# Optimization experiments

Measured on AMD Instinct MI355X. Metric: run time of the kernel, lower is better.

## Reference

```python
import jax, jax.numpy as jnp
import numpy as np

SCALE = 1000.0
NEG = -1000000000.0
B, S, T, E, H = 64, 512, 96, 256, 512  # batch, src_len, trg_len, embed_dim, hidden_dim
ENC_DIM = 2 * H


def setup_inputs() -> dict:
    key = jax.random.key(0)
    def rn(i, shape):
        return jax.random.normal(jax.random.fold_in(key, i), shape, jnp.float32) / np.sqrt(shape[-1])
    inp = {}
    inp["src"] = jax.random.uniform(jax.random.fold_in(key, 100), (B, S), jnp.float32, 50.0, 1500.0)
    src_len = jax.random.randint(jax.random.fold_in(key, 101), (B,), S // 2, S + 1)
    inp["src_mask"] = (jnp.arange(S)[None, :] < src_len[:, None]).astype(jnp.int32)
    trg = jax.random.uniform(jax.random.fold_in(key, 102), (B, T), jnp.float32, 50.0, 1500.0)
    inp["trg"] = trg.at[:, 0].set(0.0)  # position 0 is the start sentinel
    trg_len = jax.random.randint(jax.random.fold_in(key, 103), (B,), T // 2, T + 1)
    inp["trg_mask"] = (jnp.arange(T)[None, :] < trg_len[:, None]).astype(jnp.int32)
    shapes = {
        "enc_proj_W": (E, 1), "enc_proj_b": (E,),
        "enc_Wih_f": (4 * H, E), "enc_Whh_f": (4 * H, H), "enc_bih_f": (4 * H,), "enc_bhh_f": (4 * H,),
        "enc_Wih_b": (4 * H, E), "enc_Whh_b": (4 * H, H), "enc_bih_b": (4 * H,), "enc_bhh_b": (4 * H,),
        "fc_h_W": (H, 2 * H), "fc_h_b": (H,), "fc_c_W": (H, 2 * H), "fc_c_b": (H,),
        "dec_proj_W": (E, 1), "dec_proj_b": (E,),
        "attn_Wenc": (H, ENC_DIM), "attn_Wdec": (H, H), "attn_v": (1, H),
        "dec_Wih": (4 * H, E + ENC_DIM), "dec_Whh": (4 * H, H), "dec_bih": (4 * H,), "dec_bhh": (4 * H,),
        "val_W": (1, H + ENC_DIM + E), "val_b": (1,),
        "stop_W": (1, H + ENC_DIM + E), "stop_b": (1,),
    }
    for i, (name, shp) in enumerate(shapes.items()):
        inp[name] = rn(i, shp)
    return inp


def _lstm_scan(x_tbe, m_tb1, Wih, Whh, bih, bhh, reverse):
    # Mask-gated LSTM scan == pack_padded_sequence semantics (padding at end):
    # state is frozen and outputs zeroed at padded steps; reverse=True gives the
    # backward direction of the bidirectional encoder.
    b, h = x_tbe.shape[1], Whh.shape[1]
    init = (jnp.zeros((b, h), x_tbe.dtype), jnp.zeros((b, h), x_tbe.dtype))
    bias = bih + bhh
    def step(carry, xm):
        hprev, cprev = carry
        xt, m = xm
        gates = xt @ Wih.T + hprev @ Whh.T + bias  # [B,4H], torch gate order i,f,g,o
        i, f, g, o = jnp.split(gates, 4, axis=-1)
        c_new = jax.nn.sigmoid(f) * cprev + jax.nn.sigmoid(i) * jnp.tanh(g)
        h_new = jax.nn.sigmoid(o) * jnp.tanh(c_new)
        hn = jnp.where(m, h_new, hprev)
        cn = jnp.where(m, c_new, cprev)
        return (hn, cn), jnp.where(m, h_new, 0.0)
    (hT, cT), outs = jax.lax.scan(step, init, (x_tbe, m_tb1), reverse=reverse)
    return outs, hT, cT


def _forward(src, trg, enc_proj_W, enc_proj_b, enc_Wih_f, enc_Whh_f, enc_bih_f, enc_bhh_f, enc_Wih_b, enc_Whh_b, enc_bih_b, enc_bhh_b, fc_h_W, fc_h_b, fc_c_W, fc_c_b, dec_proj_W, dec_proj_b, attn_Wenc, attn_Wdec, attn_v, dec_Wih, dec_Whh, dec_bih, dec_bhh, val_W, val_b, stop_W, stop_b, src_mask, trg_mask):
    src_norm = src / SCALE
    # ---- encoder (bidirectional, n_layers=1, dropout inactive in eval) ----
    emb = src_norm[..., None] * enc_proj_W[:, 0] + enc_proj_b  # Linear(1,E) -> [B,S,E]
    emb_t = jnp.transpose(emb, (1, 0, 2))                      # [S,B,E] time-major
    m_t = (src_mask.T > 0)[..., None]                          # [S,B,1]
    out_f, hF, cF = _lstm_scan(emb_t, m_t, enc_Wih_f, enc_Whh_f, enc_bih_f, enc_bhh_f, False)
    out_b, hB, cB = _lstm_scan(emb_t, m_t, enc_Wih_b, enc_Whh_b, enc_bih_b, enc_bhh_b, True)
    enc_outputs = jnp.transpose(jnp.concatenate([out_f, out_b], -1), (1, 0, 2))  # [B,S,2H]
    hidden = jnp.tanh(jnp.concatenate([hF, hB], -1) @ fc_h_W.T + fc_h_b)  # [B,H]
    cell = jnp.tanh(jnp.concatenate([cF, cB], -1) @ fc_c_W.T + fc_c_b)    # [B,H]
    # ---- decoder loop (full teacher forcing, ratio=1.0) ----
    eh = enc_outputs @ attn_Wenc.T  # [B,S,H], loop-invariant (same math, hoisted)
    valid = src_mask > 0            # [B,S]
    dec_bias = dec_bih + dec_bhh
    def dec_step(carry, x_t):
        h, c = carry
        energy = jnp.tanh((h @ attn_Wdec.T)[:, None, :] + eh)  # [B,S,H]
        scores = jnp.where(valid, energy @ attn_v[0], NEG)     # [B,S]
        w = jax.nn.softmax(scores, axis=1)
        context = jnp.einsum('bs,bse->be', w, enc_outputs)     # [B,2H]
        e = x_t[:, None] * dec_proj_W[:, 0] + dec_proj_b       # [B,E]
        gates = jnp.concatenate([e, context], -1) @ dec_Wih.T + h @ dec_Whh.T + dec_bias
        i, f, g, o = jnp.split(gates, 4, axis=-1)
        c_new = jax.nn.sigmoid(f) * c + jax.nn.sigmoid(i) * jnp.tanh(g)
        h_new = jax.nn.sigmoid(o) * jnp.tanh(c_new)
        feat = jnp.concatenate([h_new, context, e], -1)        # [B, H+2H+E]
        pv = feat @ val_W[0] + val_b[0]
        sl = feat @ stop_W[0] + stop_b[0]
        return (h_new, c_new), (pv * SCALE, sl)
    dec_in = (trg[:, :-1] / SCALE).T  # [T-1,B]: inputs for steps t=1..trg_len-1
    _, (pred_values, stop_logits) = jax.lax.scan(dec_step, (hidden, cell), dec_in)
    return pred_values.T, stop_logits.T  # each [B, T-1]


def reference(src, src_mask, trg, trg_mask, enc_proj_W, enc_proj_b, enc_Wih_f, enc_Whh_f, enc_bih_f, enc_bhh_f, enc_Wih_b, enc_Whh_b, enc_bih_b, enc_bhh_b, fc_h_W, fc_h_b, fc_c_W, fc_c_b, dec_proj_W, dec_proj_b, attn_Wenc, attn_Wdec, attn_v, dec_Wih, dec_Whh, dec_bih, dec_bhh, val_W, val_b, stop_W, stop_b):
    return _forward(src, trg, enc_proj_W, enc_proj_b, enc_Wih_f, enc_Whh_f, enc_bih_f, enc_bhh_f, enc_Wih_b, enc_Whh_b, enc_bih_b, enc_bhh_b, fc_h_W, fc_h_b, fc_c_W, fc_c_b, dec_proj_W, dec_proj_b, attn_Wenc, attn_Wdec, attn_v, dec_Wih, dec_Whh, dec_bih, dec_bhh, val_W, val_b, stop_W, stop_b, src_mask, trg_mask)
```

## Files before the change

kernel.cpp:

```cpp
#include <hip/hip_runtime.h>
#include <hip/hip_bf16.h>

#define AGENT __HIP_MEMORY_SCOPE_AGENT

typedef float f32x4 __attribute__((ext_vector_type(4)));
typedef short short8 __attribute__((ext_vector_type(8)));
union V16 { f32x4 f; short8 s; };


__device__ __forceinline__ float sigm(float x){ return 1.f/(1.f+__expf(-x)); }
__device__ __forceinline__ float tanhfast(float x){
  float ax = fabsf(x);
  float e = __expf(-2.f*ax);
  float r = (1.f-e)/(1.f+e);
  return copysignf(r, x);
}
__device__ __forceinline__ float dot4(float4 a, float4 b){
  return fmaf(a.x,b.x, fmaf(a.y,b.y, fmaf(a.z,b.z, a.w*b.w)));
}
__device__ __forceinline__ unsigned short bfbits(float x){
  return __bfloat16_as_ushort(__float2bfloat16(x));
}
__device__ __forceinline__ float bfu2f(unsigned short u){
  union{unsigned v; float f;} x; x.v = ((unsigned)u)<<16; return x.f;
}

__global__ void __launch_bounds__(256) precompute(
  const float* __restrict__ Wenc,
  const float* __restrict__ Wihf, const float* __restrict__ epW, const float* __restrict__ epb,
  const float* __restrict__ bihf, const float* __restrict__ bhhf,
  const float* __restrict__ Wihb, const float* __restrict__ bihb, const float* __restrict__ bhhb,
  const float* __restrict__ dWih, const float* __restrict__ dpW, const float* __restrict__ dpb,
  const float* __restrict__ dbih, const float* __restrict__ dbhh,
  const float* __restrict__ valW, const float* __restrict__ valb,
  const float* __restrict__ stopW, const float* __restrict__ stopb,
  float* __restrict__ PQ, float* __restrict__ WT, float* __restrict__ hc)
{
  const int idx = blockIdx.x*256 + threadIdx.x;
  if (idx < 524288){
    const int j = idx >> 9, n = idx & 511;
    WT[idx] = Wenc[(size_t)n*1024 + j];
  } else if (idx < 524288 + 6*2048){
    const int q = idx - 524288;
    const int set = q >> 11, j = q & 2047;
    const float* row; const float* vec; float add = 0.f;
    switch(set){
      case 0: row = Wihf + (size_t)j*256; vec = epW; break;
      case 1: row = Wihf + (size_t)j*256; vec = epb; add = bihf[j]+bhhf[j]; break;
      case 2: row = Wihb + (size_t)j*256; vec = epW; break;
      case 3: row = Wihb + (size_t)j*256; vec = epb; add = bihb[j]+bhhb[j]; break;
      case 4: row = dWih + (size_t)j*1280; vec = dpW; break;
      default: row = dWih + (size_t)j*1280; vec = dpb; add = dbih[j]+dbhh[j]; break;
    }
    float a = add;
    for (int e=0;e<256;e++) a = fmaf(row[e], vec[e], a);
    PQ[set*2048 + j] = a;
  } else if (idx < 524288 + 6*2048 + 4){
    const int q = idx - (524288 + 6*2048);
    const float* wrow = (q<2) ? valW : stopW;
    const float* vec  = (q&1) ? dpb : dpW;
    float a = (q&1) ? ((q<2)? valb[0] : stopb[0]) : 0.f;
    for (int e=0;e<256;e++) a = fmaf(wrow[1536+e], vec[e], a);
    hc[q] = a;
  }
}

__global__ void __launch_bounds__(512) wconv(
  const float* __restrict__ Whhf, const float* __restrict__ Whhb,
  const float* __restrict__ dWih, const float* __restrict__ dWhh,
  const float* __restrict__ Wdec, const float* __restrict__ Wenc,
  unsigned short* __restrict__ Wbf, unsigned short* __restrict__ Wcat,
  unsigned short* __restrict__ Wdecb, unsigned short* __restrict__ Wencb)
{
  const int i = blockIdx.x*512 + threadIdx.x;
  if (i < 2097152){
    const float v = (i < 1048576) ? Whhf[i] : Whhb[i-1048576];
    Wbf[i] = bfbits(v);
  } else if (i < 2097152+3145728){
    const int q = i - 2097152;
    const int r = q/1536, k = q - r*1536;
    const float v = (k<1024) ? dWih[(size_t)r*1280 + 256 + k] : dWhh[(size_t)r*512 + (k-1024)];
    Wcat[q] = bfbits(v);
  } else if (i < 2097152+3145728+262144){
    const int q = i - (2097152+3145728);
    Wdecb[q] = bfbits(Wdec[q]);
  } else if (i < 2097152+3145728+262144+524288){
    const int q = i - (2097152+3145728+262144);
    Wencb[q] = bfbits(Wenc[q]);
  }
}

__global__ void __launch_bounds__(512) enc_mfma(
    const float* __restrict__ src, const int* __restrict__ smask,
    const unsigned short* __restrict__ Wbf,
    const float* __restrict__ PQ,
    unsigned short* __restrict__ hbuf,
    float* __restrict__ hfin,
    float* __restrict__ cf, float* __restrict__ cb,
    __hip_bfloat16* __restrict__ enc,
    unsigned* __restrict__ cnt)
{
  __shared__ float hlds[16*256];
  __shared__ float red[4*64*4];
  __shared__ float gbuf[4*256];
  __shared__ alignas(16) unsigned short hstage[256];
  __shared__ alignas(16) unsigned short estage[256];

  const int tid = threadIdx.x;
  const int bid = blockIdx.x;
  const int dir = bid>>7, bhalf = (bid>>5)&3, us = bid&31;
  const int b0 = bhalf*16;
  unsigned* gcnt = cnt + (dir*4 + bhalf)*32;
  const int wv = tid>>6, lane = tid&63;
  const int nt = wv&3, kh = wv>>2;
  const int rowb = lane&15;

  short8 bfr[8];
  {
    const int g = nt*512 + us*16 + (lane&15);
    const unsigned short* wp = Wbf + ((size_t)dir*2048 + g)*512 + kh*256 + (lane>>4)*8;
    #pragma unroll
    for (int kt=0;kt<8;kt++) bfr[kt] = *(const short8*)(wp + kt*32);
  }

  float p0=0,p1=0,p2=0,p3=0,q0=0,q1=0,q2=0,q3=0;
  float creg = 0.f, hprev = 0.f;
  int bg = 0, ug = 0;
  if (tid < 256){
    bg = b0 + (tid>>4);
    ug = us*16 + (tid&15);
    const float* P = PQ + dir*4096; const float* Q = P + 2048;
    p0=P[ug]; p1=P[ug+512]; p2=P[ug+1024]; p3=P[ug+1536];
    q0=Q[ug]; q1=Q[ug+512]; q2=Q[ug+1024]; q3=Q[ug+1536];
  }

  for (int tt=0; tt<512; ++tt){
    const int t = dir ? (511-tt) : tt;
    if (tt>0){
      if (tid==0){
        while (__hip_atomic_load(gcnt, __ATOMIC_RELAXED, AGENT) < 32u*(unsigned)tt)
          __builtin_amdgcn_s_sleep(1);
      }
      __syncthreads();
      const int par = (tt-1)&1;
      f32x4 tmp0, tmp1;
      {
        const int f0 = tid, f1 = 512 + tid;
        const unsigned short* g0 = hbuf + (((size_t)(dir*2+par)*64 + b0 + (f0>>6))<<9) + (f0&63)*8;
        const unsigned short* g1 = hbuf + (((size_t)(dir*2+par)*64 + b0 + (f1>>6))<<9) + (f1&63)*8;
        asm volatile("global_load_dwordx4 %0, %1, off sc0 sc1" : "=v"(tmp0) : "v"(g0) : "memory");
        asm volatile("global_load_dwordx4 %0, %1, off sc0 sc1" : "=v"(tmp1) : "v"(g1) : "memory");
      }
      asm volatile("s_waitcnt vmcnt(0)" ::: "memory");
      __builtin_amdgcn_sched_barrier(0);
      {
        const int r0 = tid>>6, c0 = tid&63;
        *(f32x4*)&hlds[r0*256 + ((c0 ^ (r0&7))<<2)] = tmp0;
        const int r1 = (512+tid)>>6, c1 = tid&63;
        *(f32x4*)&hlds[r1*256 + ((c1 ^ (r1&7))<<2)] = tmp1;
      }
      __syncthreads();
    }

    f32x4 acc = {0.f,0.f,0.f,0.f};
    if (tt>0){
      #pragma unroll
      for (int kt=0; kt<8; ++kt){
        const int ch = (kh*8 + kt)*4 + (lane>>4);
        V16 a; a.f = *(const f32x4*)&hlds[rowb*256 + ((ch ^ (rowb&7))<<2)];
        acc = __builtin_amdgcn_mfma_f32_16x16x32_bf16(a.s, bfr[kt], acc, 0, 0, 0);
      }
    }
    if (kh==1) *(f32x4*)&red[(nt*64+lane)*4] = acc;
    __syncthreads();
    if (kh==0){
      const f32x4 o = *(const f32x4*)&red[(nt*64+lane)*4];
      #pragma unroll
      for (int i=0;i<4;i++){
        const int r = (lane>>4)*4 + i, c = lane&15;
        gbuf[nt*256 + r*16 + c] = acc[i] + o[i];
      }
    }
    __syncthreads();

    if (tid < 256){
      const float sx = src[bg*512+t]*0.001f;
      const int m = smask[bg*512+t];
      const float gi = gbuf[0*256+tid] + sx*p0 + q0;
      const float gf = gbuf[1*256+tid] + sx*p1 + q1;
      const float gg = gbuf[2*256+tid] + sx*p2 + q2;
      const float go = gbuf[3*256+tid] + sx*p3 + q3;
      const float cn = fmaf(sigm(gf), creg, sigm(gi)*tanhfast(gg));
      const float hn = sigm(go)*tanhfast(cn);
      const float hk = m ? hn : hprev;
      creg = m ? cn : creg;
      hprev = hk;
      hstage[tid] = bfbits(hk);
      estage[tid] = bfbits(m ? hn : 0.f);
    }
    __syncthreads();
    if (tid < 32){
      const int row = tid>>1, hw = tid&1;
      const f32x4 v = *(const f32x4*)(hstage + row*16 + hw*8);
      unsigned short* dst = hbuf + (((size_t)(dir*2+(tt&1))*64 + b0 + row)<<9) + us*16 + hw*8;
      asm volatile("global_store_dwordx4 %0, %1, off sc0 sc1" :: "v"(dst), "v"(v) : "memory");
    } else if (tid < 64){
      const int j = tid-32, row = j>>1, hw = j&1;
      const f32x4 v = *(const f32x4*)(estage + row*16 + hw*8);
      *(f32x4*)((unsigned short*)enc + ((size_t)((b0+row)*512 + t))*1024 + dir*512 + us*16 + hw*8) = v;
    }
    asm volatile("s_waitcnt vmcnt(0)" ::: "memory");
    __syncthreads();
    if (tid==0) __hip_atomic_fetch_add(gcnt, 1u, __ATOMIC_RELAXED, AGENT);
  }

  if (tid < 256){
    hfin[dir*32768 + bg*512 + ug] = hprev;
    (dir ? cb : cf)[bg*512 + ug] = creg;
  }
}

__global__ void __launch_bounds__(256) fc_init(
  const float* __restrict__ hf0, const float* __restrict__ hb0,
  const float* __restrict__ cf, const float* __restrict__ cb,
  const float* __restrict__ fchW, const float* __restrict__ fchB,
  const float* __restrict__ fccW, const float* __restrict__ fccB,
  float* __restrict__ dech, float* __restrict__ decc)
{
  const int which = blockIdx.x >> 7;
  const int wid = blockIdx.x & 127;
  const int b = threadIdx.x >> 2, ul = threadIdx.x & 3;
  const int u = wid*4 + ul;
  const float* s0 = which ? cf : hf0;
  const float* s1 = which ? cb : hb0;
  const float* W = which ? fccW : fchW;
  float acc = (which ? fccB : fchB)[u];
  const float4* x0 = (const float4*)(s0 + b*512);
  const float4* x1 = (const float4*)(s1 + b*512);
  const float4* wr = (const float4*)(W + (size_t)u*1024);
  #pragma unroll 4
  for (int k=0;k<128;k++) acc += dot4(x0[k], wr[k]);
  #pragma unroll 4
  for (int k=0;k<128;k++) acc += dot4(x1[k], wr[128+k]);
  (which ? decc : dech)[b*512+u] = tanhfast(acc);
}

__global__ void __launch_bounds__(256) eh_mfma(
  const unsigned short* __restrict__ enc,
  const unsigned short* __restrict__ Wencb,
  unsigned short* __restrict__ eh2)
{
  const int b = blockIdx.x>>6, st = (blockIdx.x>>3)&7, nt0 = blockIdx.x&7;
  const int wv = threadIdx.x>>6, lane = threadIdx.x&63;
  const int sA = st*64 + wv*16 + (lane&15);
  const int kb = (lane>>4)*8;
  const unsigned short* ap  = enc + ((size_t)(b*512 + sA))*1024 + kb;
  const unsigned short* bp0 = Wencb + ((size_t)(nt0*64 + (lane&15)))*1024 + kb;
  f32x4 acc[4] = {{0,0,0,0},{0,0,0,0},{0,0,0,0},{0,0,0,0}};
  for (int k0=0; k0<1024; k0+=32){
    V16 a; a.f = *(const f32x4*)(ap + k0);
    #pragma unroll
    for (int nt=0; nt<4; ++nt){
      V16 bb; bb.f = *(const f32x4*)(bp0 + (size_t)nt*16*1024 + k0);
      acc[nt] = __builtin_amdgcn_mfma_f32_16x16x32_bf16(a.s, bb.s, acc[nt], 0, 0, 0);
    }
  }
  const int sO = st*64 + wv*16 + (lane>>4)*4;
  const int col = lane&15;
  #pragma unroll
  for (int nt=0; nt<4; ++nt){
    #pragma unroll
    for (int i=0;i<4;i++){
      eh2[((size_t)(b*512 + sO + i))*512 + nt0*64 + nt*16 + col] = bfbits(acc[nt][i]);
    }
  }
}

__global__ void __launch_bounds__(256) enc_tr(
  const unsigned short* __restrict__ enc, unsigned short* __restrict__ encT2)
{
  __shared__ unsigned short tl[64][80];
  const int b = blockIdx.x>>7, st = (blockIdx.x>>4)&7, jt = blockIdx.x&15;
  const int r = threadIdx.x>>2, q = threadIdx.x&3;
  const unsigned short* src = enc + ((size_t)(b*512 + st*64 + r))*1024 + jt*64 + q*16;
  *(short8*)&tl[r][q*16]   = *(const short8*)src;
  *(short8*)&tl[r][q*16+8] = *(const short8*)(src+8);
  __syncthreads();
  unsigned short tmp[16];
  #pragma unroll
  for (int e=0;e<16;e++) tmp[e] = tl[q*16+e][r];
  unsigned short* dst = encT2 + ((size_t)(b*1024 + jt*64 + r))*512 + st*64 + q*16;
  *(short8*)dst     = *(short8*)&tmp[0];
  *(short8*)(dst+8) = *(short8*)&tmp[8];
}

template<int NG>
__device__ __forceinline__ void gbar(unsigned* gctr, unsigned* root, int grp, unsigned gen){
  asm volatile("s_waitcnt vmcnt(0)" ::: "memory");
  __syncthreads();
  if (threadIdx.x==0){
    const unsigned old = __hip_atomic_fetch_add(gctr + grp*32, 1u, __ATOMIC_RELAXED, AGENT);
    if (old == gen*16u - 1u)
      __hip_atomic_fetch_add(root, 1u, __ATOMIC_RELAXED, AGENT);
    while (__hip_atomic_load(root, __ATOMIC_RELAXED, AGENT) < gen*(unsigned)NG)
      __builtin_amdgcn_s_sleep(1);
  }
  __syncthreads();
}
template<int NB>
__device__ __forceinline__ void mbar(unsigned* mc, unsigned mgen){
  asm volatile("s_waitcnt vmcnt(0)" ::: "memory");
  __syncthreads();
  if (threadIdx.x==0){
    __hip_atomic_fetch_add(mc, 1u, __ATOMIC_RELAXED, AGENT);
    while (__hip_atomic_load(mc, __ATOMIC_RELAXED, AGENT) < mgen*(unsigned)NB)
      __builtin_amdgcn_s_sleep(1);
  }
  __syncthreads();
}

__global__ void __launch_bounds__(512) dec_fused256(
  const float* __restrict__ trg, const int* __restrict__ smask,
  const float* __restrict__ attnv,
  const unsigned short* __restrict__ eh2,
  const unsigned short* __restrict__ encT2,
  const unsigned short* __restrict__ Wcat,
  const unsigned short* __restrict__ Wdecb,
  const float* __restrict__ PQd, const float* __restrict__ hc,
  const float* __restrict__ valW, const float* __restrict__ stopW,
  const float* __restrict__ dech0, const float* __restrict__ decc0,
  float* __restrict__ scorep, float* __restrict__ ctxf,
  unsigned short* __restrict__ xbuf, float* __restrict__ gates,
  float* __restrict__ hcur, float* __restrict__ out,
  unsigned* __restrict__ gctr, unsigned* __restrict__ root, unsigned* __restrict__ mctr)
{
  __shared__ alignas(16) float redl[8192];
  __shared__ float vlds[512];
  __shared__ float hldsa[512];
  __shared__ float adhl[128];
  __shared__ float wlds[512];
  const int tid = threadIdx.x;
  const int bid = blockIdx.x;
  const int b = bid>>2, quad = bid&3;
  const int grp = bid>>4;
  const int lane = tid&63, wv = tid>>6;
  unsigned* mc = mctr + b*32;
  unsigned g = 0, m = 0;

  vlds[tid] = attnv[tid];

  short8 gw[6];
  if (bid < 128){
    const int n = bid*16 + (lane&15);
    const unsigned short* wp = Wcat + (size_t)n*1536 + wv*192 + (lane>>4)*8;
    #pragma unroll
    for (int ks=0;ks<6;ks++) gw[ks] = *(const short8*)(wp + ks*32);
  }

  const bool isb = (quad==0);
  float hr=0.f, cr=0.f;
  float pqi=0,pqf=0,pqg=0,pqo=0, qqi=0,qqf=0,qqg=0,qqo=0;
  float vwh=0,vwc0=0,vwc1=0, swh=0,swc0=0,swc1=0;
  if (isb){
    hr = dech0[b*512+tid]; cr = decc0[b*512+tid];
    pqi = PQd[tid];      pqf = PQd[512+tid];      pqg = PQd[1024+tid];      pqo = PQd[1536+tid];
    qqi = PQd[2048+tid]; qqf = PQd[2048+512+tid]; qqg = PQd[2048+1024+tid]; qqo = PQd[2048+1536+tid];
    vwh = valW[tid]; vwc0 = valW[512+tid]; vwc1 = valW[1024+tid];
    swh = stopW[tid]; swc0 = stopW[512+tid]; swc1 = stopW[1024+tid];
  }

  if (isb){
    const unsigned hb16 = (unsigned)bfbits(hr);
    unsigned short* xp = xbuf + b*1536 + 1024 + tid;
    asm volatile("global_store_short %0, %1, off sc0 sc1" :: "v"(xp), "v"(hb16) : "memory");
    float* hp = hcur + b*512 + tid;
    asm volatile("global_store_dword %0, %1, off sc0 sc1" :: "v"(hp), "v"(hr) : "memory");
  }
  ++m; mbar<4>(mc, m);

  for (int t=0; t<95; ++t){
    {
      float hv; const float* hp = hcur + b*512 + tid;
      asm volatile("global_load_dword %0, %1, off sc0 sc1\ns_waitcnt vmcnt(0)" : "=v"(hv) : "v"(hp) : "memory");
      hldsa[tid] = hv;
      __syncthreads();
      {
        const int jl = tid>>2, uc = tid&3;
        const unsigned short* wp = Wdecb + (size_t)(quad*128 + jl)*512 + uc*128;
        float a = 0.f;
        #pragma unroll
        for (int i=0;i<16;i++){
          const short8 w8 = *(const short8*)(wp + i*8);
          #pragma unroll
          for (int e=0;e<8;e++)
            a = fmaf(hldsa[uc*128 + i*8 + e], bfu2f((unsigned short)w8[e]), a);
        }
        redl[tid] = a;
      }
      __syncthreads();
      if (tid < 128)
        adhl[tid] = redl[tid*4] + redl[tid*4+1] + redl[tid*4+2] + redl[tid*4+3];
      __syncthreads();
      {
        const unsigned short* ep = eh2 + ((size_t)(b*512 + tid))*512 + quad*128;
        float part = 0.f;
        #pragma unroll
        for (int i=0;i<16;i++){
          const short8 e8 = *(const short8*)(ep + i*8);
          #pragma unroll
          for (int e=0;e<8;e++){
            const int n = i*8 + e;
            part = fmaf(vlds[quad*128+n], tanhfast(adhl[n] + bfu2f((unsigned short)e8[e])), part);
          }
        }
        float* sp = scorep + (size_t)bid*512 + tid;
        asm volatile("global_store_dword %0, %1, off sc0 sc1" :: "v"(sp), "v"(part) : "memory");
      }
    }
    ++m; mbar<4>(mc, m);

    {
      float pa, pb, pc, pd;
      const float* pp = scorep + (size_t)(b*4)*512 + tid;
      asm volatile("global_load_dword %0, %1, off sc0 sc1" : "=v"(pa) : "v"(pp) : "memory");
      asm volatile("global_load_dword %0, %1, off sc0 sc1" : "=v"(pb) : "v"(pp+512) : "memory");
      asm volatile("global_load_dword %0, %1, off sc0 sc1" : "=v"(pc) : "v"(pp+1024) : "memory");
      asm volatile("global_load_dword %0, %1, off sc0 sc1" : "=v"(pd) : "v"(pp+1536) : "memory");
      asm volatile("s_waitcnt vmcnt(0)" ::: "memory");
      __builtin_amdgcn_sched_barrier(0);
      float s0 = (pa+pb)+(pc+pd);
      s0 = smask[b*512+tid] ? s0 : -1.0e9f;
      redl[512+tid] = s0;
      __syncthreads();
      for (int off=256; off>0; off>>=1){
        if (tid<off) redl[512+tid] = fmaxf(redl[512+tid], redl[512+tid+off]);
        __syncthreads();
      }
      const float mx = redl[512];
      __syncthreads();
      const float e = __expf(s0 - mx);
      redl[512+tid] = e;
      __syncthreads();
      for (int off=256; off>0; off>>=1){
        if (tid<off) redl[512+tid] += redl[512+tid+off];
        __syncthreads();
      }
      const float Z = redl[512];
      __syncthreads();
      wlds[tid] = e / Z;
      __syncthreads();
      {
        const int jj = tid>>1, sh = tid&1;
        const unsigned short* cp = encT2 + ((size_t)(b*1024 + quad*256 + jj))*512 + sh*256;
        float c = 0.f;
        #pragma unroll
        for (int i=0;i<32;i++){
          const short8 c8 = *(const short8*)(cp + i*8);
          #pragma unroll
          for (int e2=0;e2<8;e2++)
            c = fmaf(wlds[sh*256 + i*8 + e2], bfu2f((unsigned short)c8[e2]), c);
        }
        redl[tid] = c;
      }
      __syncthreads();
      if (tid < 256){
        const float cv = redl[tid*2] + redl[tid*2+1];
        const int j = quad*256 + tid;
        float* cp2 = ctxf + b*1024 + j;
        asm volatile("global_store_dword %0, %1, off sc0 sc1" :: "v"(cp2), "v"(cv) : "memory");
        const unsigned cb16 = (unsigned)bfbits(cv);
        unsigned short* xp = xbuf + b*1536 + j;
        asm volatile("global_store_short %0, %1, off sc0 sc1" :: "v"(xp), "v"(cb16) : "memory");
      }
    }
    ++g; gbar<16>(gctr, root, grp, g);

    if (bid < 128){
      f32x4 av[2][6];
      f32x4 acc[4] = {{0,0,0,0},{0,0,0,0},{0,0,0,0},{0,0,0,0}};
      {
        const unsigned short* xp0 = xbuf + (size_t)(lane&15)*1536 + wv*192 + (lane>>4)*8;
        #pragma unroll
        for (int ks=0;ks<6;ks++){
          const unsigned short* p = xp0 + ks*32;
          asm volatile("global_load_dwordx4 %0, %1, off sc0 sc1" : "=v"(av[0][ks]) : "v"(p) : "memory");
        }
      }
      #pragma unroll
      for (int mt=0; mt<4; ++mt){
        if (mt<3){
          const unsigned short* xpn = xbuf + (size_t)((mt+1)*16 + (lane&15))*1536 + wv*192 + (lane>>4)*8;
          #pragma unroll
          for (int ks=0;ks<6;ks++){
            const unsigned short* p = xpn + ks*32;
            asm volatile("global_load_dwordx4 %0, %1, off sc0 sc1" : "=v"(av[(mt+1)&1][ks]) : "v"(p) : "memory");
          }
          asm volatile("s_waitcnt vmcnt(6)" ::: "memory");
        } else {
          asm volatile("s_waitcnt vmcnt(0)" ::: "memory");
        }
        __builtin_amdgcn_sched_barrier(0);
        #pragma unroll
        for (int ks=0;ks<6;ks++){
          V16 a; a.f = av[mt&1][ks];
          acc[mt] = __builtin_amdgcn_mfma_f32_16x16x32_bf16(a.s, gw[ks], acc[mt], 0, 0, 0);
        }
      }
      #pragma unroll
      for (int mt=0; mt<4; ++mt)
        *(f32x4*)&redl[wv*1024 + lane*16 + mt*4] = acc[mt];
    }
    __syncthreads();
    if (bid < 128){
      #pragma unroll
      for (int h2=0; h2<2; ++h2){
        const int o = h2*512 + tid;
        const int ob = o>>4, col = o&15;
        const int mt = ob>>4, row = ob&15;
        const int base = (((row>>2)<<4) | col)*16 + mt*4 + (row&3);
        float gsum = 0.f;
        #pragma unroll
        for (int w2=0; w2<8; ++w2) gsum += redl[w2*1024 + base];
        float* gp = gates + ob*2048 + bid*16 + col;
        asm volatile("global_store_dword %0, %1, off sc0 sc1" :: "v"(gp), "v"(gsum) : "memory");
      }
    }
    ++g; gbar<16>(gctr, root, grp, g);

    if (isb){
      float g4[4], c0v, c1v;
      {
        const float* gp = gates + b*2048 + tid;
        const float* cp = ctxf + b*1024 + tid;
        asm volatile("global_load_dword %0, %1, off sc0 sc1" : "=v"(g4[0]) : "v"(gp) : "memory");
        asm volatile("global_load_dword %0, %1, off sc0 sc1" : "=v"(g4[1]) : "v"(gp+512) : "memory");
        asm volatile("global_load_dword %0, %1, off sc0 sc1" : "=v"(g4[2]) : "v"(gp+1024) : "memory");
        asm volatile("global_load_dword %0, %1, off sc0 sc1" : "=v"(g4[3]) : "v"(gp+1536) : "memory");
        asm volatile("global_load_dword %0, %1, off sc0 sc1" : "=v"(c0v) : "v"(cp) : "memory");
        asm volatile("global_load_dword %0, %1, off sc0 sc1" : "=v"(c1v) : "v"(cp+512) : "memory");
        asm volatile("s_waitcnt vmcnt(0)" ::: "memory");
        __builtin_amdgcn_sched_barrier(0);
      }
      const float x = trg[b*96 + t]*0.001f;
      const float gi = g4[0] + x*pqi + qqi;
      const float gf = g4[1] + x*pqf + qqf;
      const float gg = g4[2] + x*pqg + qqg;
      const float go = g4[3] + x*pqo + qqo;
      const float cn = fmaf(sigm(gf), cr, sigm(gi)*tanhfast(gg));
      const float hn = sigm(go)*tanhfast(cn);
      cr = cn; hr = hn;
      const unsigned hb16 = (unsigned)bfbits(hn);
      unsigned short* xp = xbuf + b*1536 + 1024 + tid;
      asm volatile("global_store_short %0, %1, off sc0 sc1" :: "v"(xp), "v"(hb16) : "memory");
      float* hp = hcur + b*512 + tid;
      asm volatile("global_store_dword %0, %1, off sc0 sc1" :: "v"(hp), "v"(hn) : "memory");
      redl[512+tid]  = fmaf(hn, vwh, fmaf(c0v, vwc0, c1v*vwc1));
      redl[1024+tid] = fmaf(hn, swh, fmaf(c0v, swc0, c1v*swc1));
      __syncthreads();
      for (int off=256; off>0; off>>=1){
        if (tid<off){ redl[512+tid]+=redl[512+tid+off]; redl[1024+tid]+=redl[1024+tid+off]; }
        __syncthreads();
      }
      if (tid==0){
        out[b*95 + t] = (redl[512] + x*hc[0] + hc[1])*1000.f;
        out[6080 + b*95 + t] = redl[1024] + x*hc[2] + hc[3];
      }
    }
    ++m; mbar<4>(mc, m);
  }
}

__global__ void __launch_bounds__(512, 4) dec_fused512(
  const float* __restrict__ trg, const int* __restrict__ smask,
  const float* __restrict__ attnv,
  const unsigned short* __restrict__ eh2,
  const unsigned short* __restrict__ encT2,
  const unsigned short* __restrict__ Wcat,
  const unsigned short* __restrict__ Wdecb,
  const float* __restrict__ PQd, const float* __restrict__ hc,
  const float* __restrict__ valW, const float* __restrict__ stopW,
  const float* __restrict__ dech0, const float* __restrict__ decc0,
  float* __restrict__ scorep, float* __restrict__ ctxf,
  unsigned short* __restrict__ xbuf, float* __restrict__ gates,
  float* __restrict__ hcur, float* __restrict__ out,
  unsigned* __restrict__ gctr, unsigned* __restrict__ root, unsigned* __restrict__ mctr)
{
  __shared__ alignas(16) float redl[8192];
  __shared__ float vlds[512];
  __shared__ float hldsa[512];
  __shared__ float adhl[64];
  __shared__ float wlds[512];
  const int tid = threadIdx.x;
  const int bid = blockIdx.x;
  const int b = bid>>3, oct = bid&7;
  const int grp = bid>>4;
  const int lane = tid&63, wv = tid>>6;
  unsigned* mc = mctr + b*32;
  unsigned g = 0, m = 0;

  vlds[tid] = attnv[tid];

  short8 gw[6];
  if (bid < 128){
    const int n = bid*16 + (lane&15);
    const unsigned short* wp = Wcat + (size_t)n*1536 + wv*192 + (lane>>4)*8;
    #pragma unroll
    for (int ks=0;ks<6;ks++) gw[ks] = *(const short8*)(wp + ks*32);
  }

  const bool isb = (oct==0);
  float hr=0.f, cr=0.f;
  float pqi=0,pqf=0,pqg=0,pqo=0, qqi=0,qqf=0,qqg=0,qqo=0;
  float vwh=0,vwc0=0,vwc1=0, swh=0,swc0=0,swc1=0;
  if (isb){
    hr = dech0[b*512+tid]; cr = decc0[b*512+tid];
    pqi = PQd[tid];      pqf = PQd[512+tid];      pqg = PQd[1024+tid];      pqo = PQd[1536+tid];
    qqi = PQd[2048+tid]; qqf = PQd[2048+512+tid]; qqg = PQd[2048+1024+tid]; qqo = PQd[2048+1536+tid];
    vwh = valW[tid]; vwc0 = valW[512+tid]; vwc1 = valW[1024+tid];
    swh = stopW[tid]; swc0 = stopW[512+tid]; swc1 = stopW[1024+tid];
  }

  if (isb){
    const unsigned hb16 = (unsigned)bfbits(hr);
    unsigned short* xp = xbuf + b*1536 + 1024 + tid;
    asm volatile("global_store_short %0, %1, off sc0 sc1" :: "v"(xp), "v"(hb16) : "memory");
    float* hp = hcur + b*512 + tid;
    asm volatile("global_store_dword %0, %1, off sc0 sc1" :: "v"(hp), "v"(hr) : "memory");
  }
  ++m; mbar<8>(mc, m);

  for (int t=0; t<95; ++t){
    {
      float hv; const float* hp = hcur + b*512 + tid;
      asm volatile("global_load_dword %0, %1, off sc0 sc1\ns_waitcnt vmcnt(0)" : "=v"(hv) : "v"(hp) : "memory");
      hldsa[tid] = hv;
      __syncthreads();
      {
        const int jl = tid>>3, uc = tid&7;
        const unsigned short* wp = Wdecb + (size_t)(oct*64 + jl)*512 + uc*64;
        float a = 0.f;
        #pragma unroll
        for (int i=0;i<8;i++){
          const short8 w8 = *(const short8*)(wp + i*8);
          #pragma unroll
          for (int e=0;e<8;e++)
            a = fmaf(hldsa[uc*64 + i*8 + e], bfu2f((unsigned short)w8[e]), a);
        }
        redl[tid] = a;
      }
      __syncthreads();
      if (tid < 64){
        float s8 = 0.f;
        #pragma unroll
        for (int i=0;i<8;i++) s8 += redl[tid*8+i];
        adhl[tid] = s8;
      }
      __syncthreads();
      {
        const unsigned short* ep = eh2 + ((size_t)(b*512 + tid))*512 + oct*64;
        float part = 0.f;
        #pragma unroll
        for (int i=0;i<8;i++){
          const short8 e8 = *(const short8*)(ep + i*8);
          #pragma unroll
          for (int e=0;e<8;e++){
            const int n = i*8 + e;
            part = fmaf(vlds[oct*64+n], tanhfast(adhl[n] + bfu2f((unsigned short)e8[e])), part);
          }
        }
        float* sp = scorep + (size_t)bid*512 + tid;
        asm volatile("global_store_dword %0, %1, off sc0 sc1" :: "v"(sp), "v"(part) : "memory");
      }
    }
    ++m; mbar<8>(mc, m);

    {
      float ps[8];
      const float* pp = scorep + (size_t)(b*8)*512 + tid;
      #pragma unroll
      for (int i=0;i<8;i++){
        const float* p = pp + i*512;
        asm volatile("global_load_dword %0, %1, off sc0 sc1" : "=v"(ps[i]) : "v"(p) : "memory");
      }
      asm volatile("s_waitcnt vmcnt(0)" ::: "memory");
      __builtin_amdgcn_sched_barrier(0);
      float s0 = ((ps[0]+ps[1])+(ps[2]+ps[3]))+((ps[4]+ps[5])+(ps[6]+ps[7]));
      s0 = smask[b*512+tid] ? s0 : -1.0e9f;
      redl[512+tid] = s0;
      __syncthreads();
      for (int off=256; off>0; off>>=1){
        if (tid<off) redl[512+tid] = fmaxf(redl[512+tid], redl[512+tid+off]);
        __syncthreads();
      }
      const float mx = redl[512];
      __syncthreads();
      const float e = __expf(s0 - mx);
      redl[512+tid] = e;
      __syncthreads();
      for (int off=256; off>0; off>>=1){
        if (tid<off) redl[512+tid] += redl[512+tid+off];
        __syncthreads();
      }
      const float Z = redl[512];
      __syncthreads();
      wlds[tid] = e / Z;
      __syncthreads();
      {
        const int jj = tid>>2, sh = tid&3;
        const unsigned short* cp = encT2 + ((size_t)(b*1024 + oct*128 + jj))*512 + sh*128;
        float c = 0.f;
        #pragma unroll
        for (int i=0;i<16;i++){
          const short8 c8 = *(const short8*)(cp + i*8);
          #pragma unroll
          for (int e2=0;e2<8;e2++)
            c = fmaf(wlds[sh*128 + i*8 + e2], bfu2f((unsigned short)c8[e2]), c);
        }
        redl[tid] = c;
      }
      __syncthreads();
      if (tid < 128){
        const float cv = redl[tid*4] + redl[tid*4+1] + redl[tid*4+2] + redl[tid*4+3];
        const int j = oct*128 + tid;
        float* cp2 = ctxf + b*1024 + j;
        asm volatile("global_store_dword %0, %1, off sc0 sc1" :: "v"(cp2), "v"(cv) : "memory");
        const unsigned cb16 = (unsigned)bfbits(cv);
        unsigned short* xp = xbuf + b*1536 + j;
        asm volatile("global_store_short %0, %1, off sc0 sc1" :: "v"(xp), "v"(cb16) : "memory");
      }
    }
    ++g; gbar<32>(gctr, root, grp, g);

    if (bid < 128){
      f32x4 av[2][6];
      f32x4 acc[4] = {{0,0,0,0},{0,0,0,0},{0,0,0,0},{0,0,0,0}};
      {
        const unsigned short* xp0 = xbuf + (size_t)(lane&15)*1536 + wv*192 + (lane>>4)*8;
        #pragma unroll
        for (int ks=0;ks<6;ks++){
          const unsigned short* p = xp0 + ks*32;
          asm volatile("global_load_dwordx4 %0, %1, off sc0 sc1" : "=v"(av[0][ks]) : "v"(p) : "memory");
        }
      }
      #pragma unroll
      for (int mt=0; mt<4; ++mt){
        if (mt<3){
          const unsigned short* xpn = xbuf + (size_t)((mt+1)*16 + (lane&15))*1536 + wv*192 + (lane>>4)*8;
          #pragma unroll
          for (int ks=0;ks<6;ks++){
            const unsigned short* p = xpn + ks*32;
            asm volatile("global_load_dwordx4 %0, %1, off sc0 sc1" : "=v"(av[(mt+1)&1][ks]) : "v"(p) : "memory");
          }
          asm volatile("s_waitcnt vmcnt(6)" ::: "memory");
        } else {
          asm volatile("s_waitcnt vmcnt(0)" ::: "memory");
        }
        __builtin_amdgcn_sched_barrier(0);
        #pragma unroll
        for (int ks=0;ks<6;ks++){
          V16 a; a.f = av[mt&1][ks];
          acc[mt] = __builtin_amdgcn_mfma_f32_16x16x32_bf16(a.s, gw[ks], acc[mt], 0, 0, 0);
        }
      }
      #pragma unroll
      for (int mt=0; mt<4; ++mt)
        *(f32x4*)&redl[wv*1024 + lane*16 + mt*4] = acc[mt];
    }
    __syncthreads();
    if (bid < 128){
      #pragma unroll
      for (int h2=0; h2<2; ++h2){
        const int o = h2*512 + tid;
        const int ob = o>>4, col = o&15;
        const int mt = ob>>4, row = ob&15;
        const int base = (((row>>2)<<4) | col)*16 + mt*4 + (row&3);
        float gsum = 0.f;
        #pragma unroll
        for (int w2=0; w2<8; ++w2) gsum += redl[w2*1024 + base];
        float* gp = gates + ob*2048 + bid*16 + col;
        asm volatile("global_store_dword %0, %1, off sc0 sc1" :: "v"(gp), "v"(gsum) : "memory");
      }
    }
    ++g; gbar<32>(gctr, root, grp, g);

    if (isb){
      float g4[4], c0v, c1v;
      {
        const float* gp = gates + b*2048 + tid;
        const float* cp = ctxf + b*1024 + tid;
        asm volatile("global_load_dword %0, %1, off sc0 sc1" : "=v"(g4[0]) : "v"(gp) : "memory");
        asm volatile("global_load_dword %0, %1, off sc0 sc1" : "=v"(g4[1]) : "v"(gp+512) : "memory");
        asm volatile("global_load_dword %0, %1, off sc0 sc1" : "=v"(g4[2]) : "v"(gp+1024) : "memory");
        asm volatile("global_load_dword %0, %1, off sc0 sc1" : "=v"(g4[3]) : "v"(gp+1536) : "memory");
        asm volatile("global_load_dword %0, %1, off sc0 sc1" : "=v"(c0v) : "v"(cp) : "memory");
        asm volatile("global_load_dword %0, %1, off sc0 sc1" : "=v"(c1v) : "v"(cp+512) : "memory");
        asm volatile("s_waitcnt vmcnt(0)" ::: "memory");
        __builtin_amdgcn_sched_barrier(0);
      }
      const float x = trg[b*96 + t]*0.001f;
      const float gi = g4[0] + x*pqi + qqi;
      const float gf = g4[1] + x*pqf + qqf;
      const float gg = g4[2] + x*pqg + qqg;
      const float go = g4[3] + x*pqo + qqo;
      const float cn = fmaf(sigm(gf), cr, sigm(gi)*tanhfast(gg));
      const float hn = sigm(go)*tanhfast(cn);
      cr = cn; hr = hn;
      const unsigned hb16 = (unsigned)bfbits(hn);
      unsigned short* xp = xbuf + b*1536 + 1024 + tid;
      asm volatile("global_store_short %0, %1, off sc0 sc1" :: "v"(xp), "v"(hb16) : "memory");
      float* hp = hcur + b*512 + tid;
      asm volatile("global_store_dword %0, %1, off sc0 sc1" :: "v"(hp), "v"(hn) : "memory");
      redl[512+tid]  = fmaf(hn, vwh, fmaf(c0v, vwc0, c1v*vwc1));
      redl[1024+tid] = fmaf(hn, swh, fmaf(c0v, swc0, c1v*swc1));
      __syncthreads();
      for (int off=256; off>0; off>>=1){
        if (tid<off){ redl[512+tid]+=redl[512+tid+off]; redl[1024+tid]+=redl[1024+tid+off]; }
        __syncthreads();
      }
      if (tid==0){
        out[b*95 + t] = (redl[512] + x*hc[0] + hc[1])*1000.f;
        out[6080 + b*95 + t] = redl[1024] + x*hc[2] + hc[3];
      }
    }
    ++m; mbar<8>(mc, m);
  }
}

extern "C" void kernel_launch(void* const* d_in, const int* in_sizes, int n_in,
                              void* d_out, int out_size, void* d_ws, size_t ws_size,
                              hipStream_t stream)
{
  (void)in_sizes; (void)n_in; (void)out_size; (void)ws_size;
  const float* src   = (const float*)d_in[0];
  const int*   smask = (const int*)  d_in[1];
  const float* trg   = (const float*)d_in[2];
  const float* epW   = (const float*)d_in[4];
  const float* epb   = (const float*)d_in[5];
  const float* Wihf  = (const float*)d_in[6];
  const float* Whhf  = (const float*)d_in[7];
  const float* bihf  = (const float*)d_in[8];
  const float* bhhf  = (const float*)d_in[9];
  const float* Wihb  = (const float*)d_in[10];
  const float* Whhb  = (const float*)d_in[11];
  const float* bihb  = (const float*)d_in[12];
  const float* bhhb  = (const float*)d_in[13];
  const float* fchW  = (const float*)d_in[14];
  const float* fchB  = (const float*)d_in[15];
  const float* fccW  = (const float*)d_in[16];
  const float* fccB  = (const float*)d_in[17];
  const float* dpW   = (const float*)d_in[18];
  const float* dpb   = (const float*)d_in[19];
  const float* Wenc  = (const float*)d_in[20];
  const float* Wdec  = (const float*)d_in[21];
  const float* attnv = (const float*)d_in[22];
  const float* dWih  = (const float*)d_in[23];
  const float* dWhh  = (const float*)d_in[24];
  const float* dbih  = (const float*)d_in[25];
  const float* dbhh  = (const float*)d_in[26];
  const float* valW  = (const float*)d_in[27];
  const float* valb  = (const float*)d_in[28];
  const float* stopW = (const float*)d_in[29];
  const float* stopb = (const float*)d_in[30];
  float* out = (float*)d_out;

  char* ws = (char*)d_ws;
  size_t off = 0;
  auto take = [&](size_t nbytes) -> char* {
    char* p = ws + off;
    off += (nbytes + 255) & ~(size_t)255;
    return p;
  };
  unsigned short* enc   = (unsigned short*)take((size_t)64*512*1024*2);
  unsigned short* eh2   = (unsigned short*)take((size_t)64*512*512*2);
  unsigned short* encT2 = (unsigned short*)take((size_t)64*1024*512*2);
  unsigned short* hbuf  = (unsigned short*)take(2*2*64*512*2);
  unsigned short* Wbf   = (unsigned short*)take((size_t)2*2048*512*2);
  unsigned short* Wcat  = (unsigned short*)take((size_t)2048*1536*2);
  unsigned short* Wdecb = (unsigned short*)take(512*512*2);
  unsigned short* Wencb = (unsigned short*)take(512*1024*2);
  float* WT    = (float*)take((size_t)1024*512*4);
  float* hfin  = (float*)take(2*64*512*4);
  float* cf    = (float*)take(64*512*4);
  float* cb    = (float*)take(64*512*4);
  float* PQ    = (float*)take(6*2048*4);
  float* dech0 = (float*)take(64*512*4);
  float* decc0 = (float*)take(64*512*4);
  float* scorep= (float*)take(512*512*4);
  float* ctxf  = (float*)take(64*1024*4);
  unsigned short* xbuf = (unsigned short*)take(64*1536*2);
  float* gates = (float*)take(64*2048*4);
  float* hcur  = (float*)take(64*512*4);
  float* hc    = (float*)take(256);
  unsigned* cnt  = (unsigned*)take(1024);
  unsigned* gctr = (unsigned*)take(4096);
  unsigned* root = (unsigned*)take(256);
  unsigned* mctr = (unsigned*)take(8192);
  float* PQd = PQ + 8192;
  (void)hipMemsetAsync(cnt, 0, 1024+4096+256+8192, stream);

  precompute<<<2097, 256, 0, stream>>>(Wenc, Wihf, epW, epb, bihf, bhhf, Wihb, bihb, bhhb,
                                       dWih, dpW, dpb, dbih, dbhh, valW, valb, stopW, stopb,
                                       PQ, WT, hc);
  wconv<<<11776, 512, 0, stream>>>(Whhf, Whhb, dWih, dWhh, Wdec, Wenc, Wbf, Wcat, Wdecb, Wencb);

  {
    void* args[] = { (void*)&src, (void*)&smask, (void*)&Wbf, (void*)&PQ,
                     (void*)&hbuf, (void*)&hfin, (void*)&cf, (void*)&cb, (void*)&enc, (void*)&cnt };
    (void)hipLaunchCooperativeKernel((void*)enc_mfma, dim3(256), dim3(512), args, 0, stream);
  }

  {
    const float* hfF = hfin;
    const float* hbF = hfin + 32768;
    fc_init<<<256, 256, 0, stream>>>(hfF, hbF, cf, cb, fchW, fchB, fccW, fccB, dech0, decc0);
  }
  eh_mfma<<<4096, 256, 0, stream>>>(enc, Wencb, eh2);
  enc_tr<<<8192, 256, 0, stream>>>(enc, encT2);

  {
    void* args[] = { (void*)&trg, (void*)&smask, (void*)&attnv,
                     (void*)&eh2, (void*)&encT2, (void*)&Wcat, (void*)&Wdecb,
                     (void*)&PQd, (void*)&hc, (void*)&valW, (void*)&stopW,
                     (void*)&dech0, (void*)&decc0,
                     (void*)&scorep, (void*)&ctxf,
                     (void*)&xbuf, (void*)&gates, (void*)&hcur, (void*)&out,
                     (void*)&gctr, (void*)&root, (void*)&mctr };
    int nb2 = 0;
    (void)hipOccupancyMaxActiveBlocksPerMultiprocessor(&nb2, dec_fused512, 512, 0);
    hipError_t e512 = hipErrorUnknown;
    if (nb2 >= 2)
      e512 = hipLaunchCooperativeKernel((void*)dec_fused512, dim3(512), dim3(512), args, 0, stream);
    if (e512 != hipSuccess)
      (void)hipLaunchCooperativeKernel((void*)dec_fused256, dim3(256), dim3(512), args, 0, stream);
  }
}
```

Before: 7.061 ms.

## Cache encoder keys in LDS, prefetch context rows, skip masked chunks, atomic gate reduction

Each decoder block now loads its slice of the projected encoder keys (eh2) into shared memory once, transposed, so later timesteps read the attention keys from LDS instead of global memory. The source length is computed from the mask once, and context-vector chunks that lie wholly beyond it are skipped, with the first half of each context row prefetched before the softmax reductions. The per-wave MFMA partial sums are reduced through LDS atomicAdd into a single 1024-float buffer rather than an 8-way strided sum, which shrinks shared memory so the large eh2 cache fits. The cost is 64KB of LDS per block, which may lower occupancy, plus LDS atomic contention. The change also assumes the mask is a contiguous prefix.

```diff
diff --git a/kernel.cpp b/kernel.cpp
--- a/kernel.cpp
+++ b/kernel.cpp
@@ -585,11 +585,11 @@
   float* __restrict__ hcur, float* __restrict__ out,
   unsigned* __restrict__ gctr, unsigned* __restrict__ root, unsigned* __restrict__ mctr)
 {
-  __shared__ alignas(16) float redl[8192];
+  __shared__ unsigned short eh2l[32768];
+  __shared__ alignas(16) float redl[2048];
   __shared__ float vlds[512];
-  __shared__ float hldsa[512];
   __shared__ float adhl[64];
-  __shared__ float wlds[512];
+  __shared__ int slen_sh;
   const int tid = threadIdx.x;
   const int bid = blockIdx.x;
   const int b = bid>>3, oct = bid&7;
@@ -599,6 +599,30 @@
   unsigned g = 0, m = 0;
 
   vlds[tid] = attnv[tid];
+
+  redl[tid] = (float)smask[b*512+tid];
+  __syncthreads();
+  for (int off=256; off>0; off>>=1){
+    if (tid<off) redl[tid] += redl[tid+off];
+    __syncthreads();
+  }
+  if (tid==0) slen_sh = (int)(redl[0]+0.5f);
+  __syncthreads();
+  const int slen = slen_sh;
+  const int nch = (slen + 127) >> 7;
+
+  {
+    const unsigned short* ep = eh2 + ((size_t)(b*512 + tid))*512 + oct*64;
+    short8 r8[8];
+    #pragma unroll
+    for (int i=0;i<8;i++) r8[i] = *(const short8*)(ep + i*8);
+    #pragma unroll
+    for (int i=0;i<8;i++)
+      #pragma unroll
+      for (int e=0;e<8;e++)
+        eh2l[(i*8+e)*512 + tid] = (unsigned short)r8[i][e];
+  }
+  __syncthreads();
 
   short8 gw[6];
   if (bid < 128){
@@ -633,7 +657,7 @@
     {
       float hv; const float* hp = hcur + b*512 + tid;
       asm volatile("global_load_dword %0, %1, off sc0 sc1\ns_waitcnt vmcnt(0)" : "=v"(hv) : "v"(hp) : "memory");
-      hldsa[tid] = hv;
+      redl[1024+tid] = hv;
       __syncthreads();
       {
         const int jl = tid>>3, uc = tid&7;
@@ -644,7 +668,7 @@
           const short8 w8 = *(const short8*)(wp + i*8);
           #pragma unroll
           for (int e=0;e<8;e++)
-            a = fmaf(hldsa[uc*64 + i*8 + e], bfu2f((unsigned short)w8[e]), a);
+            a = fmaf(redl[1024 + uc*64 + i*8 + e], bfu2f((unsigned short)w8[e]), a);
         }
         redl[tid] = a;
       }
@@ -657,17 +681,10 @@
       }
       __syncthreads();
       {
-        const unsigned short* ep = eh2 + ((size_t)(b*512 + tid))*512 + oct*64;
         float part = 0.f;
-        #pragma unroll
-        for (int i=0;i<8;i++){
-          const short8 e8 = *(const short8*)(ep + i*8);
-          #pragma unroll
-          for (int e=0;e<8;e++){
-            const int n = i*8 + e;
-            part = fmaf(vlds[oct*64+n], tanhfast(adhl[n] + bfu2f((unsigned short)e8[e])), part);
-          }
-        }
+        #pragma unroll 8
+        for (int n=0;n<64;++n)
+          part = fmaf(vlds[oct*64+n], tanhfast(adhl[n] + bfu2f(eh2l[n*512 + tid])), part);
         float* sp = scorep + (size_t)bid*512 + tid;
         asm volatile("global_store_dword %0, %1, off sc0 sc1" :: "v"(sp), "v"(part) : "memory");
       }
@@ -682,10 +699,20 @@
         const float* p = pp + i*512;
         asm volatile("global_load_dword %0, %1, off sc0 sc1" : "=v"(ps[i]) : "v"(p) : "memory");
       }
-      asm volatile("s_waitcnt vmcnt(0)" ::: "memory");
+      const int jj = tid>>2, sh = tid&3;
+      const bool act = (sh < nch);
+      const int she = act ? sh : 0;
+      const unsigned short* cp = encT2 + ((size_t)(b*1024 + oct*128 + jj))*512 + she*128;
+      f32x4 pre[8];
+      #pragma unroll
+      for (int i=0;i<8;i++){
+        const unsigned short* p = cp + i*8;
+        asm volatile("global_load_dwordx4 %0, %1, off" : "=v"(pre[i]) : "v"(p) : "memory");
+      }
+      asm volatile("s_waitcnt vmcnt(8)" ::: "memory");
       __builtin_amdgcn_sched_barrier(0);
       float s0 = ((ps[0]+ps[1])+(ps[2]+ps[3]))+((ps[4]+ps[5])+(ps[6]+ps[7]));
-      s0 = smask[b*512+tid] ? s0 : -1.0e9f;
+      s0 = (tid < slen) ? s0 : -1.0e9f;
       redl[512+tid] = s0;
       __syncthreads();
       for (int off=256; off>0; off>>=1){
@@ -703,21 +730,27 @@
       }
       const float Z = redl[512];
       __syncthreads();
-      wlds[tid] = e / Z;
-      __syncthreads();
-      {
-        const int jj = tid>>2, sh = tid&3;
-        const unsigned short* cp = encT2 + ((size_t)(b*1024 + oct*128 + jj))*512 + sh*128;
-        float c = 0.f;
-        #pragma unroll
-        for (int i=0;i<16;i++){
-          const short8 c8 = *(const short8*)(cp + i*8);
-          #pragma unroll
-          for (int e2=0;e2<8;e2++)
-            c = fmaf(wlds[sh*128 + i*8 + e2], bfu2f((unsigned short)c8[e2]), c);
-        }
-        redl[tid] = c;
-      }
+      redl[1024+tid] = e / Z;
+      __syncthreads();
+      float c = 0.f;
+      asm volatile("s_waitcnt vmcnt(0)" ::: "memory");
+      __builtin_amdgcn_sched_barrier(0);
+      #pragma unroll
+      for (int i=0;i<8;i++){
+        V16 x; x.f = pre[i];
+        #pragma unroll
+        for (int e2=0;e2<8;e2++)
+          c = fmaf(redl[1024 + she*128 + i*8 + e2], bfu2f((unsigned short)x.s[e2]), c);
+      }
+      #pragma unroll
+      for (int i=8;i<16;i++){
+        const short8 c8 = *(const short8*)(cp + i*8);
+        #pragma unroll
+        for (int e2=0;e2<8;e2++)
+          c = fmaf(redl[1024 + she*128 + i*8 + e2], bfu2f((unsigned short)c8[e2]), c);
+      }
+      c = act ? c : 0.f;
+      redl[tid] = c;
       __syncthreads();
       if (tid < 128){
         const float cv = redl[tid*4] + redl[tid*4+1] + redl[tid*4+2] + redl[tid*4+3];
@@ -731,6 +764,8 @@
     }
     ++g; gbar<32>(gctr, root, grp, g);
 
+    redl[tid] = 0.f; redl[512+tid] = 0.f;
+    __syncthreads();
     if (bid < 128){
       f32x4 av[2][6];
       f32x4 acc[4] = {{0,0,0,0},{0,0,0,0},{0,0,0,0},{0,0,0,0}};
@@ -764,7 +799,11 @@
       }
       #pragma unroll
       for (int mt=0; mt<4; ++mt)
-        *(f32x4*)&redl[wv*1024 + lane*16 + mt*4] = acc[mt];
+        #pragma unroll
+        for (int i=0;i<4;i++){
+          const int r = (lane>>4)*4 + i, cc = lane&15;
+          atomicAdd(&redl[(mt*16 + r)*16 + cc], acc[mt][i]);
+        }
     }
     __syncthreads();
     if (bid < 128){
@@ -772,11 +811,7 @@
       for (int h2=0; h2<2; ++h2){
         const int o = h2*512 + tid;
         const int ob = o>>4, col = o&15;
-        const int mt = ob>>4, row = ob&15;
-        const int base = (((row>>2)<<4) | col)*16 + mt*4 + (row&3);
-        float gsum = 0.f;
-        #pragma unroll
-        for (int w2=0; w2<8; ++w2) gsum += redl[w2*1024 + base];
+        const float gsum = redl[o];
         float* gp = gates + ob*2048 + bid*16 + col;
         asm volatile("global_store_dword %0, %1, off sc0 sc1" :: "v"(gp), "v"(gsum) : "memory");
       }
```

Result: no change. 7.093 ms (+0.5%).
